# Kernel tuning notes

Measured on AMD Instinct MI355X. Metric: run time of the kernel, lower is better.

Reference implementation:

```python
import jax, jax.numpy as jnp
import numpy as np

B = 65536   # batch
HS = 8      # max hand size
E = 12      # card embed dim
A = 20      # max actions
KC = 4      # max cards per action (padded with 0)
NH, HD = 4, 3  # MHA heads, head dim (12/4)


def _xavier(k, out_dim, in_dim, gain):
    lim = gain * np.sqrt(6.0 / (in_dim + out_dim))
    return jax.random.uniform(k, (out_dim, in_dim), jnp.float32, -lim, lim)


def setup_inputs() -> dict:
    key = jax.random.key(0)
    ks = jax.random.split(key, 32)
    card_emb = 0.1 * jax.random.normal(ks[0], (54, E), jnp.float32)
    card_emb = card_emb.at[0].set(0.0)  # padding_idx=0
    enemy_emb = 0.1 * jax.random.normal(ks[1], (54, E), jnp.float32)
    enemy_emb = enemy_emb.at[0].set(0.0)
    inp = {
        'hand_cards': jax.random.randint(ks[2], (B, HS), 0, 54),
        'game_state': jax.random.normal(ks[3], (B, 12), jnp.float32),
        'discard_pile_cards': jax.random.uniform(ks[4], (B, 54), jnp.float32),
        'enemy_card': jax.random.randint(ks[5], (B, 1), 0, 54),
        'hand_size': jax.random.randint(ks[6], (B,), 1, HS + 1),
        'action_card_indices': jax.random.randint(ks[7], (A, KC), 0, 54),
        'num_valid_actions': 20,
        'card_emb': card_emb,
        'enemy_emb': enemy_emb,
        'in_w': _xavier(ks[8], 3 * E, E, 0.5),   # MHA in_proj (torch layout [3E,E])
        'in_b': jnp.zeros((3 * E,), jnp.float32),
        'out_w': _xavier(ks[9], E, E, 0.5),
        'out_b': jnp.zeros((E,), jnp.float32),
        'gs_w1': _xavier(ks[10], 64, 12, 0.8), 'gs_b1': jnp.zeros((64,)),
        'gs_w2': _xavier(ks[11], 6, 64, 0.8), 'gs_b2': jnp.zeros((6,)),
        'dp_w1': _xavier(ks[12], 64, 54, 0.8), 'dp_b1': jnp.zeros((64,)),
        'dp_w2': _xavier(ks[13], 6, 64, 0.8), 'dp_b2': jnp.zeros((6,)),
        'ctx_w1': _xavier(ks[14], 128, 36, 0.8), 'ctx_b1': jnp.zeros((128,)),
        'ctx_w2': _xavier(ks[15], 128, 128, 0.8), 'ctx_b2': jnp.zeros((128,)),
        'sc_w1': _xavier(ks[16], 32, 140, 0.8), 'sc_b1': jnp.zeros((32,)),
        'sc_w2': _xavier(ks[17], 1, 32, 0.8), 'sc_b2': jnp.zeros((1,)),
    }
    return inp


def reference(hand_cards, game_state, discard_pile_cards, enemy_card, hand_size,
              action_card_indices, num_valid_actions,
              card_emb, enemy_emb, in_w, in_b, out_w, out_b,
              gs_w1, gs_b1, gs_w2, gs_b2, dp_w1, dp_b1, dp_w2, dp_b2,
              ctx_w1, ctx_b1, ctx_w2, ctx_b2, sc_w1, sc_b1, sc_w2, sc_b2):
    b = hand_cards.shape[0]
    # hand embeddings + self-attention with key padding mask (card 0 = pad)
    he = card_emb[hand_cards]                                  # [B,8,12]
    mask = hand_cards != 0                                     # [B,8]
    qkv = he @ in_w.T + in_b                                   # [B,8,36]
    q, k, v = jnp.split(qkv, 3, axis=-1)
    hsplit = lambda t: t.reshape(b, HS, NH, HD)
    s = jnp.einsum('bqhd,bkhd->bhqk', hsplit(q), hsplit(k)) / np.sqrt(HD)
    s = jnp.where(mask[:, None, None, :], s, -1e9)
    attn = jax.nn.softmax(s, axis=-1)
    att = jnp.einsum('bhqk,bkhd->bqhd', attn, hsplit(v)).reshape(b, HS, E)
    att = att @ out_w.T + out_b                                # [B,8,12]
    lengths = jnp.maximum(hand_size.astype(jnp.float32), 1.0)[:, None]
    hand_ctx = att.sum(axis=1) / lengths                       # [B,12]
    # enemy / game-state / discard encoders (eval mode: dropout off)
    en = enemy_emb[enemy_card[:, 0]]                           # [B,12]
    g = jax.nn.relu(game_state @ gs_w1.T + gs_b1) @ gs_w2.T + gs_b2        # [B,6]
    d = jax.nn.relu(discard_pile_cards @ dp_w1.T + dp_b1) @ dp_w2.T + dp_b2  # [B,6]
    ctx = jnp.concatenate([hand_ctx, en, g, d], axis=-1)       # [B,36]
    ctx = jax.nn.relu(ctx @ ctx_w1.T + ctx_b1) @ ctx_w2.T + ctx_b2         # [B,128]
    # ragged per-action card lists: masked mean of card embeddings
    aemb = card_emb[action_card_indices]                       # [A,K,12]
    am = (action_card_indices != 0).astype(jnp.float32)[..., None]
    cnt = jnp.maximum(am.sum(axis=1), 1.0)
    arep = (aemb * am).sum(axis=1) / cnt                       # [A,12]
    feat = jnp.concatenate([
        jnp.broadcast_to(ctx[:, None, :], (b, A, ctx.shape[-1])),
        jnp.broadcast_to(arep[None], (b, A, E)),
    ], axis=-1)                                                # [B,A,140]
    sc = (jax.nn.relu(feat @ sc_w1.T + sc_b1) @ sc_w2.T + sc_b2)[..., 0]   # [B,A]
    valid = jnp.arange(A) < num_valid_actions
    return jnp.where(valid[None, :], sc, -1e8)
```

## Files before the change

kernel.cpp:

```cpp
#include <hip/hip_runtime.h>
#include <hip/hip_bf16.h>
#include <math.h>

#define HS 8
#define E 12
#define NA 20
#define KC 4

typedef float f32x4 __attribute__((ext_vector_type(4)));
typedef short short8 __attribute__((ext_vector_type(8)));

__device__ float g_ET[4 * 54 * 54];
__device__ float g_VT[4 * 54 * 4];
__device__ float g_abias[NA * 32];
__device__ __align__(16) short g_gsB[4 * 64 * 16];
__device__ __align__(16) short g_dpB[8 * 64 * 16];
__device__ __align__(16) short g_ctxB[16 * 64 * 16];
__device__ __align__(16) short g_WtB[8 * 64 * 16];
__device__ __align__(16) float g_feat[65536 * 32];

__device__ __forceinline__ short bfh(float f) {
    return (short)__bfloat16_as_ushort(__float2bfloat16(f));
}
__device__ __forceinline__ void split_bf16(float f, short& hi, short& lo) {
    hi = bfh(f);
    float fh = __uint_as_float(((unsigned)(unsigned short)hi) << 16);
    lo = bfh(f - fh);
}
__device__ __forceinline__ void split8(const float* x, short8& hi, short8& lo) {
#pragma unroll
    for (int j = 0; j < 8; ++j) {
        short h, l;
        split_bf16(x[j], h, l);
        hi[j] = h; lo[j] = l;
    }
}

#define MFMA(a, b, c) __builtin_amdgcn_mfma_f32_16x16x32_bf16(a, b, c, 0, 0, 0)

__device__ __forceinline__ f32x4 mfma3v(short8 ah, short8 al, short8 bh, short8 bl,
                                        f32x4 c) {
    c = MFMA(ah, bh, c);
    c = MFMA(ah, bl, c);
    c = MFMA(al, bh, c);
    return c;
}

__device__ float ctxw(int hid, int k, const float* ctx_w1, const float* out_w,
                      const float* out_b) {
    if (k < 12) {
        float s = 0.f;
        for (int i = 0; i < 12; ++i) s += ctx_w1[hid * 36 + i] * out_w[i * 12 + k];
        return s;
    } else if (k < 24) {
        return ctx_w1[hid * 36 + k];
    } else if (k == 24) {
        float s = 0.f;
        for (int i = 0; i < 12; ++i) s += ctx_w1[hid * 36 + i] * out_b[i];
        return 8.f * s;
    } else if (k < 32) {
        return 0.f;
    } else if (k < 44) {
        return ctx_w1[hid * 36 + 24 + (k - 32)];
    }
    return 0.f;
}

__global__ void precompute_kernel(const float* __restrict__ card_emb,
                                  const int* __restrict__ aci,
                                  const float* __restrict__ ctx_w2,
                                  const float* __restrict__ ctx_b2,
                                  const float* __restrict__ sc_w1,
                                  const float* __restrict__ sc_b1,
                                  const float* __restrict__ in_w,
                                  const float* __restrict__ in_b,
                                  const float* __restrict__ ctx_w1,
                                  const float* __restrict__ dp_w1,
                                  const float* __restrict__ gs_w1,
                                  const float* __restrict__ out_w,
                                  const float* __restrict__ out_b) {
    const int O_ET = 11664, O_VT = O_ET + 216, O_GS = O_VT + 2048, O_DP = O_GS + 4096;
    const int O_CX = O_DP + 8192, O_WT = O_CX + 4096, O_AB = O_WT + 640;
    int t = blockIdx.x * 256 + threadIdx.x;
    if (t < O_ET) {
        int h = t / 2916, rem = t % 2916;
        int c1 = rem / 54, c2 = rem % 54;
        float s = 0.f;
#pragma unroll
        for (int d = 0; d < 3; ++d) {
            float q = in_b[h * 3 + d], k = in_b[12 + h * 3 + d];
            for (int j = 0; j < 12; ++j) {
                q += in_w[(h * 3 + d) * 12 + j] * card_emb[c1 * 12 + j];
                k += in_w[(12 + h * 3 + d) * 12 + j] * card_emb[c2 * 12 + j];
            }
            s += q * k;
        }
        g_ET[t] = expf(s * 0.5773502691896258f);
    } else if (t < O_VT) {
        int t2 = t - O_ET;
        int h = t2 / 54, c = t2 % 54;
#pragma unroll
        for (int d = 0; d < 3; ++d) {
            float v = in_b[24 + h * 3 + d];
            for (int j = 0; j < 12; ++j)
                v += in_w[(24 + h * 3 + d) * 12 + j] * card_emb[c * 12 + j];
            g_VT[t2 * 4 + d] = v;
        }
        g_VT[t2 * 4 + 3] = 1.0f;
    } else if (t < O_GS) {
        int id = t - O_VT;
        int tt = id >> 9, lane = (id >> 3) & 63, j = id & 7;
        int g = lane >> 4, n = lane & 15;
        int k = 8 * g + j, col = 16 * tt + n;
        float wv = (k < 12) ? gs_w1[col * 12 + k] : 0.f;
        short hi, lo;
        split_bf16(wv, hi, lo);
        int base = ((tt << 6) + lane) << 4;
        g_gsB[base + j] = hi;
        g_gsB[base + 8 + j] = lo;
    } else if (t < O_DP) {
        int id = t - O_GS;
        int st = id >> 9, lane = (id >> 3) & 63, j = id & 7;
        int s = st >> 2, tt = st & 3;
        int g = lane >> 4, n = lane & 15;
        int k = 32 * s + 8 * g + j, col = 16 * tt + n;
        float wv = (k < 54) ? dp_w1[col * 54 + k] : 0.f;
        short hi, lo;
        split_bf16(wv, hi, lo);
        int base = ((st << 6) + lane) << 4;
        g_dpB[base + j] = hi;
        g_dpB[base + 8 + j] = lo;
    } else if (t < O_CX) {
        int id = t - O_DP;
        int st = id >> 9, lane = (id >> 3) & 63, j = id & 7;
        int s = st >> 3, tt = st & 7;
        int g = lane >> 4, n = lane & 15;
        int k = 32 * s + 8 * g + j, hid = 16 * tt + n;
        float wv = ctxw(hid, k, ctx_w1, out_w, out_b);
        short hi, lo;
        split_bf16(wv, hi, lo);
        int base = ((st << 6) + lane) << 4;
        g_ctxB[base + j] = hi;
        g_ctxB[base + 8 + j] = lo;
    } else if (t < O_WT) {
        int id = t - O_CX;
        int st = id >> 9, lane = (id >> 3) & 63, j = id & 7;
        int s = st >> 1, tt = st & 1;
        int g = lane >> 4, n = lane & 15;
        int k = 32 * s + 8 * g + j, col = 16 * tt + n;
        float wv = 0.f;
        for (int i = 0; i < 128; ++i) wv += sc_w1[col * 140 + i] * ctx_w2[i * 128 + k];
        short hi, lo;
        split_bf16(wv, hi, lo);
        int base = ((st << 6) + lane) << 4;
        g_WtB[base + j] = hi;
        g_WtB[base + 8 + j] = lo;
    } else if (t < O_AB) {
        int t2 = t - O_WT;
        int a = t2 >> 5, j = t2 & 31;
        float arep[E];
#pragma unroll
        for (int k2 = 0; k2 < E; ++k2) arep[k2] = 0.f;
        float cnt = 0.f;
#pragma unroll
        for (int c = 0; c < KC; ++c) {
            int idx = aci[a * KC + c];
            if (idx != 0) {
                cnt += 1.f;
#pragma unroll
                for (int k2 = 0; k2 < E; ++k2) arep[k2] += card_emb[idx * E + k2];
            }
        }
        float inv = 1.f / fmaxf(cnt, 1.f);
        float s = sc_b1[j];
#pragma unroll
        for (int k2 = 0; k2 < E; ++k2) s += sc_w1[j * 140 + 128 + k2] * (arep[k2] * inv);
        for (int i = 0; i < 128; ++i) s += sc_w1[j * 140 + i] * ctx_b2[i];
        g_abias[t2] = s;
    }
}

__global__ __launch_bounds__(1024) void featA_kernel(
    const int* __restrict__ hand_cards, const int* __restrict__ enemy_card,
    const int* __restrict__ hand_size, const float* __restrict__ enemy_emb) {
    __shared__ float sET[4 * 54 * 54];
    __shared__ __align__(16) float4 sV[4 * 54];
    __shared__ float sEN[54 * 12];

    int tid = threadIdx.x;
    for (int i = tid; i < 11664; i += 1024) sET[i] = g_ET[i];
    for (int i = tid; i < 864; i += 1024) ((float*)sV)[i] = g_VT[i];
    for (int i = tid; i < 648; i += 1024) sEN[i] = enemy_emb[i];
    __syncthreads();

    int q = tid & 3;
    int el = tid >> 2;
    int b = blockIdx.x * 256 + el;

    int hc[HS];
    {
        const int4* hp = (const int4*)(hand_cards + (size_t)b * HS);
        int4 h0 = hp[0], h1 = hp[1];
        hc[0] = h0.x; hc[1] = h0.y; hc[2] = h0.z; hc[3] = h0.w;
        hc[4] = h1.x; hc[5] = h1.y; hc[6] = h1.z; hc[7] = h1.w;
    }
    int ec = enemy_card[b];

    float4 vv[HS];
#pragma unroll
    for (int k = 0; k < HS; ++k) {
        float4 v = sV[q * 54 + hc[k]];
        if (hc[k] == 0) v = make_float4(0.f, 0.f, 0.f, 0.f);
        vv[k] = v;
    }

    const float* eb = sET + q * 2916;
    float a0 = 0.f, a1 = 0.f, a2 = 0.f;
#pragma unroll
    for (int p = 0; p < HS; ++p) {
        const float* er = eb + hc[p] * 54;
        float n0 = 0.f, n1 = 0.f, n2 = 0.f, nw = 0.f;
#pragma unroll
        for (int k = 0; k < HS; ++k) {
            float e = er[hc[k]];
            n0 += e * vv[k].x;
            n1 += e * vv[k].y;
            n2 += e * vv[k].z;
            nw += e * vv[k].w;
        }
        float rw = 1.f / fmaxf(nw, 1e-30f);
        a0 += n0 * rw; a1 += n1 * rw; a2 += n2 * rw;
    }
    float invlen = 1.f / fmaxf((float)hand_size[b], 1.f);
    float* fr = g_feat + (size_t)b * 32;
    fr[3 * q + 0] = a0 * invlen;
    fr[3 * q + 1] = a1 * invlen;
    fr[3 * q + 2] = a2 * invlen;
    fr[12 + 3 * q + 0] = sEN[ec * 12 + 3 * q + 0];
    fr[12 + 3 * q + 1] = sEN[ec * 12 + 3 * q + 1];
    fr[12 + 3 * q + 2] = sEN[ec * 12 + 3 * q + 2];
    if (q == 0) fr[24] = invlen;
}

#define FENCE() asm volatile("s_waitcnt lgkmcnt(0)" ::: "memory")

__global__ __launch_bounds__(512, 4) void scoreB_kernel(
    const float* __restrict__ game_state, const float* __restrict__ discard,
    const int* __restrict__ num_valid, const float* __restrict__ gs_b1,
    const float* __restrict__ dp_b1, const float* __restrict__ gs_w2,
    const float* __restrict__ dp_w2, const float* __restrict__ gs_b2,
    const float* __restrict__ dp_b2, const float* __restrict__ ctx_b1,
    const float* __restrict__ sc_w2, const float* __restrict__ sc_b2,
    float* __restrict__ out) {
    __shared__ __align__(16) float sU[8 * 2112];
    __shared__ __align__(16) float sAB[NA * 36];
    __shared__ __align__(16) float sW2[32];
    __shared__ __align__(16) float sGS2T[64 * 12];
    __shared__ __align__(16) float sDPW2T[64 * 12];
    __shared__ float sCB[128];
    __shared__ float sGSB[64];
    __shared__ float sDPB[64];

    int tid = threadIdx.x;
    for (int i = tid; i < NA * 36; i += 512) {
        int a = i / 36, c = i % 36;
        sAB[i] = (c < 32) ? g_abias[a * 32 + c] : 0.f;
    }
    for (int i = tid; i < 768; i += 512) {
        int r = i / 12, c = i % 12;
        sGS2T[i] = (c < 6) ? gs_w2[c * 64 + r] : 0.f;
        sDPW2T[i] = (c < 6) ? dp_w2[c * 64 + r] : 0.f;
    }
    if (tid < 32) sW2[tid] = sc_w2[tid];
    if (tid >= 32 && tid < 160) sCB[tid - 32] = ctx_b1[tid - 32];
    if (tid >= 160 && tid < 224) sGSB[tid - 160] = gs_b1[tid - 160];
    if (tid >= 224 && tid < 288) sDPB[tid - 224] = dp_b1[tid - 224];
    for (int i = tid; i < 8 * 320; i += 512) {
        int w2 = i / 320;
        sU[w2 * 2112 + (i % 320)] = 0.f;
    }
    __syncthreads();

    int lane = tid & 63;
    int w = tid >> 6;
    int n = lane & 15, g = lane >> 4;
    size_t eb0 = (size_t)blockIdx.x * 128 + (w << 4);
    size_t bE = eb0 + n;
    float* SW = sU + w * 2112;
    float gb2 = (n < 6) ? gs_b2[n] : 0.f;
    float db2 = (n < 6) ? dp_b2[n] : 0.f;

    float fca[8];
    {
        const float4* fp = (const float4*)(g_feat + bE * 32 + 8 * g);
        float4 f0 = fp[0], f1 = fp[1];
        fca[0] = f0.x; fca[1] = f0.y; fca[2] = f0.z; fca[3] = f0.w;
        fca[4] = f1.x; fca[5] = f1.y; fca[6] = f1.z; fca[7] = f1.w;
    }

    f32x4 gacc[4], dacc[4];
    {
        short8 gah, gal, dah0, dal0, dah1, dal1;
        {
            float xg[8];
#pragma unroll
            for (int j = 0; j < 8; ++j) {
                int k = 8 * g + j;
                xg[j] = (k < 12) ? game_state[bE * 12 + k] : 0.f;
            }
            split8(xg, gah, gal);
            const float* drow = discard + bE * 54;
            float xa[8], xb[8];
            {
                const float2* p = (const float2*)(drow + 8 * g);
                float2 v0 = p[0], v1 = p[1], v2 = p[2], v3 = p[3];
                xa[0] = v0.x; xa[1] = v0.y; xa[2] = v1.x; xa[3] = v1.y;
                xa[4] = v2.x; xa[5] = v2.y; xa[6] = v3.x; xa[7] = v3.y;
            }
#pragma unroll
            for (int j = 0; j < 8; ++j) {
                int k = 32 + 8 * g + j;
                xb[j] = (k < 54) ? drow[k] : 0.f;
            }
            split8(xa, dah0, dal0);
            split8(xb, dah1, dal1);
        }
#pragma unroll
        for (int t = 0; t < 4; ++t) {
            const short8* bp = (const short8*)&g_gsB[((t << 6) + lane) << 4];
            float bv = sGSB[16 * t + n];
            f32x4 cc = {bv, bv, bv, bv};
            gacc[t] = mfma3v(gah, gal, bp[0], bp[1], cc);
        }
#pragma unroll
        for (int t = 0; t < 4; ++t) {
            const short8* b0 = (const short8*)&g_dpB[((t << 6) + lane) << 4];
            const short8* b1 = (const short8*)&g_dpB[(((4 + t) << 6) + lane) << 4];
            float bv = sDPB[16 * t + n];
            f32x4 cc = {bv, bv, bv, bv};
            cc = mfma3v(dah0, dal0, b0[0], b0[1], cc);
            dacc[t] = mfma3v(dah1, dal1, b1[0], b1[1], cc);
        }
    }

    {
        float pg[4][6], pd[4][6];
#pragma unroll
        for (int r = 0; r < 4; ++r)
#pragma unroll
            for (int c = 0; c < 6; ++c) { pg[r][c] = 0.f; pd[r][c] = 0.f; }
#pragma unroll
        for (int t = 0; t < 4; ++t) {
            const float* wg = &sGS2T[(16 * t + n) * 12];
            float4 wga = *(const float4*)wg;
            float2 wgb = *(const float2*)(wg + 4);
            const float* wd = &sDPW2T[(16 * t + n) * 12];
            float4 wda = *(const float4*)wd;
            float2 wdb = *(const float2*)(wd + 4);
#pragma unroll
            for (int r = 0; r < 4; ++r) {
                float hg = fmaxf(gacc[t][r], 0.f);
                float hd = fmaxf(dacc[t][r], 0.f);
                pg[r][0] += hg * wga.x; pg[r][1] += hg * wga.y; pg[r][2] += hg * wga.z;
                pg[r][3] += hg * wga.w; pg[r][4] += hg * wgb.x; pg[r][5] += hg * wgb.y;
                pd[r][0] += hd * wda.x; pd[r][1] += hd * wda.y; pd[r][2] += hd * wda.z;
                pd[r][3] += hd * wda.w; pd[r][4] += hd * wdb.x; pd[r][5] += hd * wdb.y;
            }
        }
#pragma unroll
        for (int r = 0; r < 4; ++r)
#pragma unroll
            for (int c = 0; c < 6; ++c) {
                float v = pg[r][c];
                v += __shfl_xor(v, 1, 64);
                v += __shfl_xor(v, 2, 64);
                v += __shfl_xor(v, 4, 64);
                v += __shfl_xor(v, 8, 64);
                pg[r][c] = v;
                float u = pd[r][c];
                u += __shfl_xor(u, 1, 64);
                u += __shfl_xor(u, 2, 64);
                u += __shfl_xor(u, 4, 64);
                u += __shfl_xor(u, 8, 64);
                pd[r][c] = u;
            }
        if (n < 6) {
#pragma unroll
            for (int r = 0; r < 4; ++r) {
                int e = 4 * g + r;
                float gv = pg[r][0];
                gv = (n == 1) ? pg[r][1] : gv; gv = (n == 2) ? pg[r][2] : gv;
                gv = (n == 3) ? pg[r][3] : gv; gv = (n == 4) ? pg[r][4] : gv;
                gv = (n == 5) ? pg[r][5] : gv;
                float dv = pd[r][0];
                dv = (n == 1) ? pd[r][1] : dv; dv = (n == 2) ? pd[r][2] : dv;
                dv = (n == 3) ? pd[r][3] : dv; dv = (n == 4) ? pd[r][4] : dv;
                dv = (n == 5) ? pd[r][5] : dv;
                SW[e * 20 + n] = gv + gb2;
                SW[e * 20 + 6 + n] = dv + db2;
            }
        }
    }
    FENCE();

    f32x4 cacc[8];
#pragma unroll
    for (int tt = 0; tt < 8; ++tt) {
        float bv = sCB[16 * tt + n];
        f32x4 cc = {bv, bv, bv, bv};
        cacc[tt] = cc;
    }
    {
        short8 ah, al;
        split8(fca, ah, al);
#pragma unroll
        for (int tt = 0; tt < 8; ++tt) {
            const short8* bp = (const short8*)&g_ctxB[((tt << 6) + lane) << 4];
            cacc[tt] = mfma3v(ah, al, bp[0], bp[1], cacc[tt]);
        }
        if (g < 2) {
            float xb[8];
#pragma unroll
            for (int j2 = 0; j2 < 4; ++j2) {
                float2 v = *(const float2*)&SW[n * 20 + 8 * g + 2 * j2];
                xb[2 * j2] = v.x;
                xb[2 * j2 + 1] = v.y;
            }
            split8(xb, ah, al);
        } else {
            short8 zz = {0, 0, 0, 0, 0, 0, 0, 0};
            ah = zz; al = zz;
        }
#pragma unroll
        for (int tt = 0; tt < 8; ++tt) {
            const short8* bp = (const short8*)&g_ctxB[(((8 + tt) << 6) + lane) << 4];
            cacc[tt] = mfma3v(ah, al, bp[0], bp[1], cacc[tt]);
        }
    }

#pragma unroll
    for (int tt = 0; tt < 8; ++tt)
#pragma unroll
        for (int r = 0; r < 4; ++r)
            SW[(4 * g + r) * 132 + 16 * tt + n] = fmaxf(cacc[tt][r], 0.f);
    FENCE();

    f32x4 uacc[2];
    {
        f32x4 z = {0.f, 0.f, 0.f, 0.f};
        uacc[0] = z; uacc[1] = z;
    }
#pragma unroll
    for (int s = 0; s < 4; ++s) {
        const float4* ap = (const float4*)&SW[n * 132 + 32 * s + 8 * g];
        float4 a0 = ap[0], a1 = ap[1];
        float ha[8] = {a0.x, a0.y, a0.z, a0.w, a1.x, a1.y, a1.z, a1.w};
        short8 ah, al;
        split8(ha, ah, al);
#pragma unroll
        for (int t2 = 0; t2 < 2; ++t2) {
            const short8* bp = (const short8*)&g_WtB[(((s * 2 + t2) << 6) + lane) << 4];
            uacc[t2] = mfma3v(ah, al, bp[0], bp[1], uacc[t2]);
        }
    }

#pragma unroll
    for (int t2 = 0; t2 < 2; ++t2)
#pragma unroll
        for (int r = 0; r < 4; ++r)
            SW[(4 * g + r) * 132 + 16 * t2 + n] = uacc[t2][r];
    FENCE();
    {
        float uu[32];
        {
            const float4* up = (const float4*)&SW[n * 132];
#pragma unroll
            for (int j8 = 0; j8 < 8; ++j8) {
                float4 v = up[j8];
                uu[4 * j8 + 0] = v.x; uu[4 * j8 + 1] = v.y;
                uu[4 * j8 + 2] = v.z; uu[4 * j8 + 3] = v.w;
            }
        }
        int nva = num_valid[0];
        float sb2 = sc_b2[0];
#pragma unroll
        for (int t = 0; t < 5; ++t) {
            int a = g * 5 + t;
            const float4* ab = (const float4*)&sAB[a * 36];
            float s = sb2;
#pragma unroll
            for (int j8 = 0; j8 < 8; ++j8) {
                float4 av = ab[j8];
                float4 wv = ((const float4*)sW2)[j8];
                s += wv.x * fmaxf(uu[4 * j8 + 0] + av.x, 0.f);
                s += wv.y * fmaxf(uu[4 * j8 + 1] + av.y, 0.f);
                s += wv.z * fmaxf(uu[4 * j8 + 2] + av.z, 0.f);
                s += wv.w * fmaxf(uu[4 * j8 + 3] + av.w, 0.f);
            }
            out[bE * NA + a] = (a < nva) ? s : -1.0e8f;
        }
    }
}

extern "C" void kernel_launch(void* const* d_in, const int* in_sizes, int n_in,
                              void* d_out, int out_size, void* d_ws, size_t ws_size,
                              hipStream_t stream) {
    const int* hand_cards = (const int*)d_in[0];
    const float* game_state = (const float*)d_in[1];
    const float* discard = (const float*)d_in[2];
    const int* enemy_card = (const int*)d_in[3];
    const int* hand_size = (const int*)d_in[4];
    const int* aci = (const int*)d_in[5];
    const int* num_valid = (const int*)d_in[6];
    const float* card_emb = (const float*)d_in[7];
    const float* enemy_emb = (const float*)d_in[8];
    const float* in_w = (const float*)d_in[9];
    const float* in_b = (const float*)d_in[10];
    const float* out_w = (const float*)d_in[11];
    const float* out_b = (const float*)d_in[12];
    const float* gs_w1 = (const float*)d_in[13];
    const float* gs_b1 = (const float*)d_in[14];
    const float* gs_w2 = (const float*)d_in[15];
    const float* gs_b2 = (const float*)d_in[16];
    const float* dp_w1 = (const float*)d_in[17];
    const float* dp_b1 = (const float*)d_in[18];
    const float* dp_w2 = (const float*)d_in[19];
    const float* dp_b2 = (const float*)d_in[20];
    const float* ctx_w1 = (const float*)d_in[21];
    const float* ctx_b1 = (const float*)d_in[22];
    const float* ctx_w2 = (const float*)d_in[23];
    const float* ctx_b2 = (const float*)d_in[24];
    const float* sc_w1 = (const float*)d_in[25];
    const float* sc_b1 = (const float*)d_in[26];
    const float* sc_w2 = (const float*)d_in[27];
    const float* sc_b2 = (const float*)d_in[28];

    int B = in_sizes[0] / HS;

    precompute_kernel<<<121, 256, 0, stream>>>(
        card_emb, aci, ctx_w2, ctx_b2, sc_w1, sc_b1, in_w, in_b, ctx_w1,
        dp_w1, gs_w1, out_w, out_b);
    featA_kernel<<<B / 256, 1024, 0, stream>>>(hand_cards, enemy_card, hand_size,
                                               enemy_emb);
    scoreB_kernel<<<B / 128, 512, 0, stream>>>(
        game_state, discard, num_valid, gs_b1, dp_b1, gs_w2, dp_w2, gs_b2, dp_b2,
        ctx_b1, sc_w2, sc_b2, (float*)d_out);
}
```

Measured before the change: 58.58 us.

## Stage MFMA weight fragments in LDS and loop four tiles per wave

scoreB now copies the pre-split bf16 hi/lo weight fragments for the gs, dp, ctx and Wt layers into shared memory once per block, instead of every wave reading them from global memory. Each wave processes four 16-row tiles in a loop, with all inputs for those tiles prefetched into registers up front. The block shrinks to 256 threads covering 256 rows, and launch bounds change to (256,1). The aim is to amortize weight loads and raise memory-level parallelism, at the cost of higher register pressure and LDS use, which may lower occupancy.

```diff
diff --git a/kernel.cpp b/kernel.cpp
--- a/kernel.cpp
+++ b/kernel.cpp
@@ -244,7 +244,7 @@
 
 #define FENCE() asm volatile("s_waitcnt lgkmcnt(0)" ::: "memory")
 
-__global__ __launch_bounds__(512, 4) void scoreB_kernel(
+__global__ __launch_bounds__(256, 1) void scoreB_kernel(
     const float* __restrict__ game_state, const float* __restrict__ discard,
     const int* __restrict__ num_valid, const float* __restrict__ gs_b1,
     const float* __restrict__ dp_b1, const float* __restrict__ gs_w2,
@@ -252,7 +252,11 @@
     const float* __restrict__ dp_b2, const float* __restrict__ ctx_b1,
     const float* __restrict__ sc_w2, const float* __restrict__ sc_b2,
     float* __restrict__ out) {
-    __shared__ __align__(16) float sU[8 * 2112];
+    __shared__ __align__(16) short sGsH[4 * 64 * 8], sGsL[4 * 64 * 8];
+    __shared__ __align__(16) short sDpH[8 * 64 * 8], sDpL[8 * 64 * 8];
+    __shared__ __align__(16) short sCxH[16 * 64 * 8], sCxL[16 * 64 * 8];
+    __shared__ __align__(16) short sWtH[8 * 64 * 8], sWtL[8 * 64 * 8];
+    __shared__ __align__(16) float sU[4 * 2112];
     __shared__ __align__(16) float sAB[NA * 36];
     __shared__ __align__(16) float sW2[32];
     __shared__ __align__(16) float sGS2T[64 * 12];
@@ -262,11 +266,30 @@
     __shared__ float sDPB[64];
 
     int tid = threadIdx.x;
-    for (int i = tid; i < NA * 36; i += 512) {
+    {
+        int4 h, l;
+        h = ((const int4*)g_gsB)[2 * tid]; l = ((const int4*)g_gsB)[2 * tid + 1];
+        ((int4*)sGsH)[tid] = h; ((int4*)sGsL)[tid] = l;
+#pragma unroll
+        for (int r = 0; r < 2; ++r) {
+            int i = tid + 256 * r;
+            h = ((const int4*)g_dpB)[2 * i]; l = ((const int4*)g_dpB)[2 * i + 1];
+            ((int4*)sDpH)[i] = h; ((int4*)sDpL)[i] = l;
+            h = ((const int4*)g_WtB)[2 * i]; l = ((const int4*)g_WtB)[2 * i + 1];
+            ((int4*)sWtH)[i] = h; ((int4*)sWtL)[i] = l;
+        }
+#pragma unroll
+        for (int r = 0; r < 4; ++r) {
+            int i = tid + 256 * r;
+            h = ((const int4*)g_ctxB)[2 * i]; l = ((const int4*)g_ctxB)[2 * i + 1];
+            ((int4*)sCxH)[i] = h; ((int4*)sCxL)[i] = l;
+        }
+    }
+    for (int i = tid; i < NA * 36; i += 256) {
         int a = i / 36, c = i % 36;
         sAB[i] = (c < 32) ? g_abias[a * 32 + c] : 0.f;
     }
-    for (int i = tid; i < 768; i += 512) {
+    for (int i = tid; i < 768; i += 256) {
         int r = i / 12, c = i % 12;
         sGS2T[i] = (c < 6) ? gs_w2[c * 64 + r] : 0.f;
         sDPW2T[i] = (c < 6) ? dp_w2[c * 64 + r] : 0.f;
@@ -274,231 +297,240 @@
     if (tid < 32) sW2[tid] = sc_w2[tid];
     if (tid >= 32 && tid < 160) sCB[tid - 32] = ctx_b1[tid - 32];
     if (tid >= 160 && tid < 224) sGSB[tid - 160] = gs_b1[tid - 160];
-    if (tid >= 224 && tid < 288) sDPB[tid - 224] = dp_b1[tid - 224];
-    for (int i = tid; i < 8 * 320; i += 512) {
-        int w2 = i / 320;
-        sU[w2 * 2112 + (i % 320)] = 0.f;
-    }
+    if (tid >= 224) sDPB[tid - 224] = dp_b1[tid - 224];
+    if (tid >= 192 && tid < 224) sDPB[tid - 160] = dp_b1[tid - 160];
     __syncthreads();
 
     int lane = tid & 63;
     int w = tid >> 6;
     int n = lane & 15, g = lane >> 4;
-    size_t eb0 = (size_t)blockIdx.x * 128 + (w << 4);
-    size_t bE = eb0 + n;
+    size_t eb0 = (size_t)blockIdx.x * 256 + (w << 6);
     float* SW = sU + w * 2112;
     float gb2 = (n < 6) ? gs_b2[n] : 0.f;
     float db2 = (n < 6) ? dp_b2[n] : 0.f;
-
-    float fca[8];
-    {
-        const float4* fp = (const float4*)(g_feat + bE * 32 + 8 * g);
-        float4 f0 = fp[0], f1 = fp[1];
-        fca[0] = f0.x; fca[1] = f0.y; fca[2] = f0.z; fca[3] = f0.w;
-        fca[4] = f1.x; fca[5] = f1.y; fca[6] = f1.z; fca[7] = f1.w;
-    }
-
-    f32x4 gacc[4], dacc[4];
-    {
-        short8 gah, gal, dah0, dal0, dah1, dal1;
-        {
-            float xg[8];
-#pragma unroll
-            for (int j = 0; j < 8; ++j) {
-                int k = 8 * g + j;
-                xg[j] = (k < 12) ? game_state[bE * 12 + k] : 0.f;
-            }
-            split8(xg, gah, gal);
-            const float* drow = discard + bE * 54;
-            float xa[8], xb[8];
+    int nva = num_valid[0];
+    float sb2 = sc_b2[0];
+
+    const short8* GsH = (const short8*)sGsH;
+    const short8* GsL = (const short8*)sGsL;
+    const short8* DpH = (const short8*)sDpH;
+    const short8* DpL = (const short8*)sDpL;
+    const short8* CxH = (const short8*)sCxH;
+    const short8* CxL = (const short8*)sCxL;
+    const short8* WtH = (const short8*)sWtH;
+    const short8* WtL = (const short8*)sWtL;
+
+    float xg[4][8], xa[4][8], xb[4][8], fc[4][8];
+#pragma unroll
+    for (int t = 0; t < 4; ++t) {
+        size_t bE = eb0 + t * 16 + n;
+#pragma unroll
+        for (int j = 0; j < 8; ++j) {
+            int k = 8 * g + j;
+            xg[t][j] = (k < 12) ? game_state[bE * 12 + k] : 0.f;
+        }
+        const float* drow = discard + bE * 54;
+        {
+            const float2* p = (const float2*)(drow + 8 * g);
+            float2 v0 = p[0], v1 = p[1], v2 = p[2], v3 = p[3];
+            xa[t][0] = v0.x; xa[t][1] = v0.y; xa[t][2] = v1.x; xa[t][3] = v1.y;
+            xa[t][4] = v2.x; xa[t][5] = v2.y; xa[t][6] = v3.x; xa[t][7] = v3.y;
+        }
+#pragma unroll
+        for (int j = 0; j < 8; ++j) {
+            int k = 32 + 8 * g + j;
+            xb[t][j] = (k < 54) ? drow[k] : 0.f;
+        }
+        {
+            const float4* fp = (const float4*)(g_feat + bE * 32 + 8 * g);
+            float4 f0 = fp[0], f1 = fp[1];
+            fc[t][0] = f0.x; fc[t][1] = f0.y; fc[t][2] = f0.z; fc[t][3] = f0.w;
+            fc[t][4] = f1.x; fc[t][5] = f1.y; fc[t][6] = f1.z; fc[t][7] = f1.w;
+        }
+    }
+
+#pragma unroll
+    for (int t = 0; t < 4; ++t) {
+        size_t bE = eb0 + t * 16 + n;
+        f32x4 gacc[4], dacc[4];
+        {
+            short8 gah, gal, dah0, dal0, dah1, dal1;
+            split8(xg[t], gah, gal);
+            split8(xa[t], dah0, dal0);
+            split8(xb[t], dah1, dal1);
+#pragma unroll
+            for (int tt = 0; tt < 4; ++tt) {
+                float bv = sGSB[16 * tt + n];
+                f32x4 cc = {bv, bv, bv, bv};
+                gacc[tt] = mfma3v(gah, gal, GsH[(tt << 6) + lane], GsL[(tt << 6) + lane], cc);
+            }
+#pragma unroll
+            for (int tt = 0; tt < 4; ++tt) {
+                float bv = sDPB[16 * tt + n];
+                f32x4 cc = {bv, bv, bv, bv};
+                cc = mfma3v(dah0, dal0, DpH[(tt << 6) + lane], DpL[(tt << 6) + lane], cc);
+                dacc[tt] = mfma3v(dah1, dal1, DpH[((4 + tt) << 6) + lane],
+                                  DpL[((4 + tt) << 6) + lane], cc);
+            }
+        }
+
+        {
+            float pg[4][6], pd[4][6];
+#pragma unroll
+            for (int r = 0; r < 4; ++r)
+#pragma unroll
+                for (int c = 0; c < 6; ++c) { pg[r][c] = 0.f; pd[r][c] = 0.f; }
+#pragma unroll
+            for (int tt = 0; tt < 4; ++tt) {
+                const float* wg = &sGS2T[(16 * tt + n) * 12];
+                float4 wga = *(const float4*)wg;
+                float2 wgb = *(const float2*)(wg + 4);
+                const float* wd = &sDPW2T[(16 * tt + n) * 12];
+                float4 wda = *(const float4*)wd;
+                float2 wdb = *(const float2*)(wd + 4);
+#pragma unroll
+                for (int r = 0; r < 4; ++r) {
+                    float hg = fmaxf(gacc[tt][r], 0.f);
+                    float hd = fmaxf(dacc[tt][r], 0.f);
+                    pg[r][0] += hg * wga.x; pg[r][1] += hg * wga.y; pg[r][2] += hg * wga.z;
+                    pg[r][3] += hg * wga.w; pg[r][4] += hg * wgb.x; pg[r][5] += hg * wgb.y;
+                    pd[r][0] += hd * wda.x; pd[r][1] += hd * wda.y; pd[r][2] += hd * wda.z;
+                    pd[r][3] += hd * wda.w; pd[r][4] += hd * wdb.x; pd[r][5] += hd * wdb.y;
+                }
+            }
+#pragma unroll
+            for (int r = 0; r < 4; ++r)
+#pragma unroll
+                for (int c = 0; c < 6; ++c) {
+                    float v = pg[r][c];
+                    v += __shfl_xor(v, 1, 64);
+                    v += __shfl_xor(v, 2, 64);
+                    v += __shfl_xor(v, 4, 64);
+                    v += __shfl_xor(v, 8, 64);
+                    pg[r][c] = v;
+                    float u = pd[r][c];
+                    u += __shfl_xor(u, 1, 64);
+                    u += __shfl_xor(u, 2, 64);
+                    u += __shfl_xor(u, 4, 64);
+                    u += __shfl_xor(u, 8, 64);
+                    pd[r][c] = u;
+                }
+            if (n < 6) {
+#pragma unroll
+                for (int r = 0; r < 4; ++r) {
+                    int e = 4 * g + r;
+                    float gv = pg[r][0];
+                    gv = (n == 1) ? pg[r][1] : gv; gv = (n == 2) ? pg[r][2] : gv;
+                    gv = (n == 3) ? pg[r][3] : gv; gv = (n == 4) ? pg[r][4] : gv;
+                    gv = (n == 5) ? pg[r][5] : gv;
+                    float dv = pd[r][0];
+                    dv = (n == 1) ? pd[r][1] : dv; dv = (n == 2) ? pd[r][2] : dv;
+                    dv = (n == 3) ? pd[r][3] : dv; dv = (n == 4) ? pd[r][4] : dv;
+                    dv = (n == 5) ? pd[r][5] : dv;
+                    SW[e * 20 + n] = gv + gb2;
+                    SW[e * 20 + 6 + n] = dv + db2;
+                }
+            } else if (n < 10) {
+#pragma unroll
+                for (int r = 0; r < 4; ++r)
+                    SW[(4 * g + r) * 20 + 6 + n] = 0.f;
+            }
+        }
+        FENCE();
+
+        f32x4 cacc[8];
+#pragma unroll
+        for (int tt = 0; tt < 8; ++tt) {
+            float bv = sCB[16 * tt + n];
+            f32x4 cc = {bv, bv, bv, bv};
+            cacc[tt] = cc;
+        }
+        {
+            short8 ah, al;
+            split8(fc[t], ah, al);
+#pragma unroll
+            for (int tt = 0; tt < 8; ++tt)
+                cacc[tt] = mfma3v(ah, al, CxH[(tt << 6) + lane], CxL[(tt << 6) + lane],
+                                  cacc[tt]);
+            if (g < 2) {
+                float xf[8];
+#pragma unroll
+                for (int j2 = 0; j2 < 4; ++j2) {
+                    float2 v = *(const float2*)&SW[n * 20 + 8 * g + 2 * j2];
+                    xf[2 * j2] = v.x;
+                    xf[2 * j2 + 1] = v.y;
+                }
+                split8(xf, ah, al);
+            } else {
+                short8 zz = {0, 0, 0, 0, 0, 0, 0, 0};
+                ah = zz; al = zz;
+            }
+#pragma unroll
+            for (int tt = 0; tt < 8; ++tt)
+                cacc[tt] = mfma3v(ah, al, CxH[((8 + tt) << 6) + lane],
+                                  CxL[((8 + tt) << 6) + lane], cacc[tt]);
+        }
+
+#pragma unroll
+        for (int tt = 0; tt < 8; ++tt)
+#pragma unroll
+            for (int r = 0; r < 4; ++r)
+                SW[(4 * g + r) * 132 + 16 * tt + n] = fmaxf(cacc[tt][r], 0.f);
+        FENCE();
+
+        f32x4 uacc[2];
+        {
+            f32x4 z = {0.f, 0.f, 0.f, 0.f};
+            uacc[0] = z; uacc[1] = z;
+        }
+#pragma unroll
+        for (int s = 0; s < 4; ++s) {
+            const float4* ap = (const float4*)&SW[n * 132 + 32 * s + 8 * g];
+            float4 a0 = ap[0], a1 = ap[1];
+            float ha[8] = {a0.x, a0.y, a0.z, a0.w, a1.x, a1.y, a1.z, a1.w};
+            short8 ah, al;
+            split8(ha, ah, al);
+#pragma unroll
+            for (int t2 = 0; t2 < 2; ++t2)
+                uacc[t2] = mfma3v(ah, al, WtH[((s * 2 + t2) << 6) + lane],
+                                  WtL[((s * 2 + t2) << 6) + lane], uacc[t2]);
+        }
+
+#pragma unroll
+        for (int t2 = 0; t2 < 2; ++t2)
+#pragma unroll
+            for (int r = 0; r < 4; ++r)
+                SW[(4 * g + r) * 132 + 16 * t2 + n] = uacc[t2][r];
+        FENCE();
+        {
+            float uu[32];
             {
-                const float2* p = (const float2*)(drow + 8 * g);
-                float2 v0 = p[0], v1 = p[1], v2 = p[2], v3 = p[3];
-                xa[0] = v0.x; xa[1] = v0.y; xa[2] = v1.x; xa[3] = v1.y;
-                xa[4] = v2.x; xa[5] = v2.y; xa[6] = v3.x; xa[7] = v3.y;
-            }
-#pragma unroll
-            for (int j = 0; j < 8; ++j) {
-                int k = 32 + 8 * g + j;
-                xb[j] = (k < 54) ? drow[k] : 0.f;
-            }
-            split8(xa, dah0, dal0);
-            split8(xb, dah1, dal1);
-        }
-#pragma unroll
-        for (int t = 0; t < 4; ++t) {
-            const short8* bp = (const short8*)&g_gsB[((t << 6) + lane) << 4];
-            float bv = sGSB[16 * t + n];
-            f32x4 cc = {bv, bv, bv, bv};
-            gacc[t] = mfma3v(gah, gal, bp[0], bp[1], cc);
-        }
-#pragma unroll
-        for (int t = 0; t < 4; ++t) {
-            const short8* b0 = (const short8*)&g_dpB[((t << 6) + lane) << 4];
-            const short8* b1 = (const short8*)&g_dpB[(((4 + t) << 6) + lane) << 4];
-            float bv = sDPB[16 * t + n];
-            f32x4 cc = {bv, bv, bv, bv};
-            cc = mfma3v(dah0, dal0, b0[0], b0[1], cc);
-            dacc[t] = mfma3v(dah1, dal1, b1[0], b1[1], cc);
-        }
-    }
-
-    {
-        float pg[4][6], pd[4][6];
-#pragma unroll
-        for (int r = 0; r < 4; ++r)
-#pragma unroll
-            for (int c = 0; c < 6; ++c) { pg[r][c] = 0.f; pd[r][c] = 0.f; }
-#pragma unroll
-        for (int t = 0; t < 4; ++t) {
-            const float* wg = &sGS2T[(16 * t + n) * 12];
-            float4 wga = *(const float4*)wg;
-            float2 wgb = *(const float2*)(wg + 4);
-            const float* wd = &sDPW2T[(16 * t + n) * 12];
-            float4 wda = *(const float4*)wd;
-            float2 wdb = *(const float2*)(wd + 4);
-#pragma unroll
-            for (int r = 0; r < 4; ++r) {
-                float hg = fmaxf(gacc[t][r], 0.f);
-                float hd = fmaxf(dacc[t][r], 0.f);
-                pg[r][0] += hg * wga.x; pg[r][1] += hg * wga.y; pg[r][2] += hg * wga.z;
-                pg[r][3] += hg * wga.w; pg[r][4] += hg * wgb.x; pg[r][5] += hg * wgb.y;
-                pd[r][0] += hd * wda.x; pd[r][1] += hd * wda.y; pd[r][2] += hd * wda.z;
-                pd[r][3] += hd * wda.w; pd[r][4] += hd * wdb.x; pd[r][5] += hd * wdb.y;
-            }
-        }
-#pragma unroll
-        for (int r = 0; r < 4; ++r)
-#pragma unroll
-            for (int c = 0; c < 6; ++c) {
-                float v = pg[r][c];
-                v += __shfl_xor(v, 1, 64);
-                v += __shfl_xor(v, 2, 64);
-                v += __shfl_xor(v, 4, 64);
-                v += __shfl_xor(v, 8, 64);
-                pg[r][c] = v;
-                float u = pd[r][c];
-                u += __shfl_xor(u, 1, 64);
-                u += __shfl_xor(u, 2, 64);
-                u += __shfl_xor(u, 4, 64);
-                u += __shfl_xor(u, 8, 64);
-                pd[r][c] = u;
-            }
-        if (n < 6) {
-#pragma unroll
-            for (int r = 0; r < 4; ++r) {
-                int e = 4 * g + r;
-                float gv = pg[r][0];
-                gv = (n == 1) ? pg[r][1] : gv; gv = (n == 2) ? pg[r][2] : gv;
-                gv = (n == 3) ? pg[r][3] : gv; gv = (n == 4) ? pg[r][4] : gv;
-                gv = (n == 5) ? pg[r][5] : gv;
-                float dv = pd[r][0];
-                dv = (n == 1) ? pd[r][1] : dv; dv = (n == 2) ? pd[r][2] : dv;
-                dv = (n == 3) ? pd[r][3] : dv; dv = (n == 4) ? pd[r][4] : dv;
-                dv = (n == 5) ? pd[r][5] : dv;
-                SW[e * 20 + n] = gv + gb2;
-                SW[e * 20 + 6 + n] = dv + db2;
-            }
-        }
-    }
-    FENCE();
-
-    f32x4 cacc[8];
-#pragma unroll
-    for (int tt = 0; tt < 8; ++tt) {
-        float bv = sCB[16 * tt + n];
-        f32x4 cc = {bv, bv, bv, bv};
-        cacc[tt] = cc;
-    }
-    {
-        short8 ah, al;
-        split8(fca, ah, al);
-#pragma unroll
-        for (int tt = 0; tt < 8; ++tt) {
-            const short8* bp = (const short8*)&g_ctxB[((tt << 6) + lane) << 4];
-            cacc[tt] = mfma3v(ah, al, bp[0], bp[1], cacc[tt]);
-        }
-        if (g < 2) {
-            float xb[8];
-#pragma unroll
-            for (int j2 = 0; j2 < 4; ++j2) {
-                float2 v = *(const float2*)&SW[n * 20 + 8 * g + 2 * j2];
-                xb[2 * j2] = v.x;
-                xb[2 * j2 + 1] = v.y;
-            }
-            split8(xb, ah, al);
-        } else {
-            short8 zz = {0, 0, 0, 0, 0, 0, 0, 0};
-            ah = zz; al = zz;
-        }
-#pragma unroll
-        for (int tt = 0; tt < 8; ++tt) {
-            const short8* bp = (const short8*)&g_ctxB[(((8 + tt) << 6) + lane) << 4];
-            cacc[tt] = mfma3v(ah, al, bp[0], bp[1], cacc[tt]);
-        }
-    }
-
-#pragma unroll
-    for (int tt = 0; tt < 8; ++tt)
-#pragma unroll
-        for (int r = 0; r < 4; ++r)
-            SW[(4 * g + r) * 132 + 16 * tt + n] = fmaxf(cacc[tt][r], 0.f);
-    FENCE();
-
-    f32x4 uacc[2];
-    {
-        f32x4 z = {0.f, 0.f, 0.f, 0.f};
-        uacc[0] = z; uacc[1] = z;
-    }
-#pragma unroll
-    for (int s = 0; s < 4; ++s) {
-        const float4* ap = (const float4*)&SW[n * 132 + 32 * s + 8 * g];
-        float4 a0 = ap[0], a1 = ap[1];
-        float ha[8] = {a0.x, a0.y, a0.z, a0.w, a1.x, a1.y, a1.z, a1.w};
-        short8 ah, al;
-        split8(ha, ah, al);
-#pragma unroll
-        for (int t2 = 0; t2 < 2; ++t2) {
-            const short8* bp = (const short8*)&g_WtB[(((s * 2 + t2) << 6) + lane) << 4];
-            uacc[t2] = mfma3v(ah, al, bp[0], bp[1], uacc[t2]);
-        }
-    }
-
-#pragma unroll
-    for (int t2 = 0; t2 < 2; ++t2)
-#pragma unroll
-        for (int r = 0; r < 4; ++r)
-            SW[(4 * g + r) * 132 + 16 * t2 + n] = uacc[t2][r];
-    FENCE();
-    {
-        float uu[32];
-        {
-            const float4* up = (const float4*)&SW[n * 132];
-#pragma unroll
-            for (int j8 = 0; j8 < 8; ++j8) {
-                float4 v = up[j8];
-                uu[4 * j8 + 0] = v.x; uu[4 * j8 + 1] = v.y;
-                uu[4 * j8 + 2] = v.z; uu[4 * j8 + 3] = v.w;
-            }
-        }
-        int nva = num_valid[0];
-        float sb2 = sc_b2[0];
-#pragma unroll
-        for (int t = 0; t < 5; ++t) {
-            int a = g * 5 + t;
-            const float4* ab = (const float4*)&sAB[a * 36];
-            float s = sb2;
-#pragma unroll
-            for (int j8 = 0; j8 < 8; ++j8) {
-                float4 av = ab[j8];
-                float4 wv = ((const float4*)sW2)[j8];
-                s += wv.x * fmaxf(uu[4 * j8 + 0] + av.x, 0.f);
-                s += wv.y * fmaxf(uu[4 * j8 + 1] + av.y, 0.f);
-                s += wv.z * fmaxf(uu[4 * j8 + 2] + av.z, 0.f);
-                s += wv.w * fmaxf(uu[4 * j8 + 3] + av.w, 0.f);
-            }
-            out[bE * NA + a] = (a < nva) ? s : -1.0e8f;
-        }
+                const float4* up = (const float4*)&SW[n * 132];
+#pragma unroll
+                for (int j8 = 0; j8 < 8; ++j8) {
+                    float4 v = up[j8];
+                    uu[4 * j8 + 0] = v.x; uu[4 * j8 + 1] = v.y;
+                    uu[4 * j8 + 2] = v.z; uu[4 * j8 + 3] = v.w;
+                }
+            }
+#pragma unroll
+            for (int ta = 0; ta < 5; ++ta) {
+                int a = g * 5 + ta;
+                const float4* ab = (const float4*)&sAB[a * 36];
+                float s = sb2;
+#pragma unroll
+                for (int j8 = 0; j8 < 8; ++j8) {
+                    float4 av = ab[j8];
+                    float4 wv = ((const float4*)sW2)[j8];
+                    s += wv.x * fmaxf(uu[4 * j8 + 0] + av.x, 0.f);
+                    s += wv.y * fmaxf(uu[4 * j8 + 1] + av.y, 0.f);
+                    s += wv.z * fmaxf(uu[4 * j8 + 2] + av.z, 0.f);
+                    s += wv.w * fmaxf(uu[4 * j8 + 3] + av.w, 0.f);
+                }
+                out[bE * NA + a] = (a < nva) ? s : -1.0e8f;
+            }
+        }
+        FENCE();
     }
 }
 
@@ -542,7 +574,7 @@
         dp_w1, gs_w1, out_w, out_b);
     featA_kernel<<<B / 256, 1024, 0, stream>>>(hand_cards, enemy_card, hand_size,
                                                enemy_emb);
-    scoreB_kernel<<<B / 128, 512, 0, stream>>>(
+    scoreB_kernel<<<B / 256, 256, 0, stream>>>(
         game_state, discard, num_valid, gs_b1, dp_b1, gs_w2, dp_w2, gs_b2, dp_b2,
         ctx_b1, sc_w2, sc_b2, (float*)d_out);
 }
```

Measured after the change: 81.48 us. 39.1% more time.
